# Optimization experiments

Measured on AMD Instinct MI355X. Metric: run time of the kernel, lower is better.

Reference implementation:

```python
import jax, jax.numpy as jnp
import numpy as np

D = 512
A = 256
MAX_DEPTH = 50.0
ANGLE_RANGE = 60.0
SIGMA = 0.5

ANGLES = jnp.linspace(-ANGLE_RANGE / 2, ANGLE_RANGE / 2, A)  # [A]
DEPTHS = jnp.linspace(0.0, MAX_DEPTH, D)                     # [D]
DEG2RAD = np.float32(np.pi / 180.0)


def _generate_prior(p):
    # p: [B, 3] = [theta_a, d, theta_p]
    d = p[:, 1]        # [B]
    theta_p = p[:, 2]  # [B]
    angle_rad = (theta_p[:, None] + ANGLES[None, :]) * DEG2RAD   # [B, A]
    d_theory = d[:, None] / jnp.cos(angle_rad)                   # [B, A]
    valid = (d_theory > 0.0) & (d_theory < MAX_DEPTH)            # [B, A]
    # Gaussian soft-binning over depth: [B, D, A]
    diff = DEPTHS[None, :, None] - d_theory[:, None, :]
    P = jnp.exp(-(diff * diff) / (2.0 * SIGMA * SIGMA))
    P = jnp.where(valid[:, None, :], P, 0.0)
    # per-column (over depth) normalization, skipping empty columns
    col_sum = P.sum(axis=1, keepdims=True)                       # [B, 1, A]
    denom = jnp.where(col_sum > 0.0, col_sum, 1.0)
    return P / denom


def setup_inputs() -> dict:
    key = jax.random.key(0)
    k1, k2, k3, k4, k5, k6 = jax.random.split(key, 6)
    B = 256

    def make_p(ka, kd, kp):
        theta_a = jax.random.uniform(ka, (B,), minval=-30.0, maxval=30.0)
        d = jax.random.uniform(kd, (B,), minval=1.0, maxval=40.0)
        theta_p = jax.random.uniform(kp, (B,), minval=-10.0, maxval=10.0)
        return jnp.stack([theta_a, d, theta_p], axis=1).astype(jnp.float32)

    return {"p": make_p(k1, k2, k3), "p_calib": make_p(k4, k5, k6)}


def reference(p, p_calib):
    P_d = _generate_prior(p)
    P_c = _generate_prior(p_calib)
    return (P_d, P_c)
```

## Files before the change

kernel.cpp:

```cpp
#include <hip/hip_runtime.h>


#define DD 512
#define AA 256

__global__ __launch_bounds__(256) void prior_kernel(const float* __restrict__ p0,
                                                    const float* __restrict__ p1,
                                                    float* __restrict__ out) {
    const int blk = blockIdx.x;
    const int b   = blk & 255;
    const float* __restrict__ pp = (blk < 256) ? p0 : p1;

    __shared__ __align__(16) float dt_s[AA];
    __shared__ __align__(16) float inv_s[AA];

    const float d  = pp[b * 3 + 1];
    const float th = pp[b * 3 + 2];

    const int t = threadIdx.x;

    {
        const int a = t;
        const float ang = -30.0f + (float)a * (60.0f / 255.0f);
        const float rad = (th + ang) * 0.017453292519943295f;
        float dt = d / cosf(rad);
        const bool valid = (dt > 0.0f) && (dt < 50.0f);
        float sum = 0.0f;
        #pragma unroll 8
        for (int j = 0; j < DD; ++j) {
            const float dep  = (float)j * (50.0f / 511.0f);
            const float diff = dep - dt;
            sum += __expf(-2.0f * diff * diff);
        }
        const float den = (sum > 0.0f) ? sum : 1.0f;
        inv_s[a] = valid ? (1.0f / den) : 0.0f;
        dt_s[a]  = valid ? dt : 1.0e9f;
    }
    __syncthreads();

    const int a4   = (t & 63) * 4;
    const int jblk = t >> 6;
    const float4 dtv = *(const float4*)&dt_s[a4];
    const float4 inv = *(const float4*)&inv_s[a4];

    float* __restrict__ outp = out + (size_t)blk * (DD * AA) + a4;
    const int j0 = jblk * (DD / 4);
    #pragma unroll 4
    for (int j = j0; j < j0 + DD / 4; ++j) {
        const float dep = (float)j * (50.0f / 511.0f);
        float4 v;
        float dx = dep - dtv.x; v.x = __expf(-2.0f * dx * dx) * inv.x;
        float dy = dep - dtv.y; v.y = __expf(-2.0f * dy * dy) * inv.y;
        float dz = dep - dtv.z; v.z = __expf(-2.0f * dz * dz) * inv.z;
        float dw = dep - dtv.w; v.w = __expf(-2.0f * dw * dw) * inv.w;
        *(float4*)(outp + (size_t)j * AA) = v;
    }
}

extern "C" void kernel_launch(void* const* d_in, const int* in_sizes, int n_in,
                              void* d_out, int out_size, void* d_ws, size_t ws_size,
                              hipStream_t stream) {
    const float* p0 = (const float*)d_in[0];
    const float* p1 = (const float*)d_in[1];
    float* out = (float*)d_out;
    prior_kernel<<<dim3(2 * 256), dim3(256), 0, stream>>>(p0, p1, out);
}
```

Before: 261.8 us.

## Window Gaussian column sums, fold normalization into exp2, zero-fill outside band

```diff
diff --git a/kernel.cpp b/kernel.cpp
--- a/kernel.cpp
+++ b/kernel.cpp
@@ -3,21 +3,32 @@
 
 #define DD 512
 #define AA 256
+#define DSTEP (50.0f / 511.0f)
+#define K2 (-2.8853900817779268f)
+#define BHW 34
+
+__device__ __forceinline__ float fexp2(float x) { return __builtin_amdgcn_exp2f(x); }
+__device__ __forceinline__ float flog2(float x) { return __builtin_amdgcn_logf(x); }
 
 __global__ __launch_bounds__(256) void prior_kernel(const float* __restrict__ p0,
                                                     const float* __restrict__ p1,
                                                     float* __restrict__ out) {
-    const int blk = blockIdx.x;
-    const int b   = blk & 255;
+    const int bh   = blockIdx.x;
+    const int blk  = bh >> 1;
+    const int half = bh & 1;
+    const int b    = blk & 255;
     const float* __restrict__ pp = (blk < 256) ? p0 : p1;
 
     __shared__ __align__(16) float dt_s[AA];
-    __shared__ __align__(16) float inv_s[AA];
+    __shared__ __align__(16) float li_s[AA];
+    __shared__ int jlo_s, jhi_s;
+
+    const int t = threadIdx.x;
+    if (t == 0) { jlo_s = 1 << 30; jhi_s = -(1 << 30); }
+    __syncthreads();
 
     const float d  = pp[b * 3 + 1];
     const float th = pp[b * 3 + 2];
-
-    const int t = threadIdx.x;
 
     {
         const int a = t;
@@ -25,36 +36,57 @@
         const float rad = (th + ang) * 0.017453292519943295f;
         float dt = d / cosf(rad);
         const bool valid = (dt > 0.0f) && (dt < 50.0f);
-        float sum = 0.0f;
-        #pragma unroll 8
-        for (int j = 0; j < DD; ++j) {
-            const float dep  = (float)j * (50.0f / 511.0f);
-            const float diff = dep - dt;
-            sum += __expf(-2.0f * diff * diff);
+        float li = 0.0f;
+        if (valid) {
+            const int c  = (int)(dt * (511.0f / 50.0f) + 0.5f);
+            const int lo = max(0, c - 32);
+            const int hi = min(DD - 1, c + 32);
+            float sum = 0.0f;
+            for (int j = lo; j <= hi; ++j) {
+                const float dep = (float)j * DSTEP;
+                const float dx  = dep - dt;
+                sum += fexp2(K2 * dx * dx);
+            }
+            li = -flog2(sum);
+            atomicMin(&jlo_s, c);
+            atomicMax(&jhi_s, c);
+        } else {
+            dt = 1.0e5f;
         }
-        const float den = (sum > 0.0f) ? sum : 1.0f;
-        inv_s[a] = valid ? (1.0f / den) : 0.0f;
-        dt_s[a]  = valid ? dt : 1.0e9f;
+        dt_s[a] = dt;
+        li_s[a] = li;
     }
     __syncthreads();
 
-    const int a4   = (t & 63) * 4;
-    const int jblk = t >> 6;
+    const int a4 = (t & 63) * 4;
     const float4 dtv = *(const float4*)&dt_s[a4];
-    const float4 inv = *(const float4*)&inv_s[a4];
+    const float4 liv = *(const float4*)&li_s[a4];
+
+    const int jq0 = half * 256 + (t >> 6) * 64;
+    const int jq1 = jq0 + 64;
+    const int lo = max(jq0, min(jq1, jlo_s - BHW));
+    const int hi = max(lo,  min(jq1, jhi_s + BHW + 1));
 
     float* __restrict__ outp = out + (size_t)blk * (DD * AA) + a4;
-    const int j0 = jblk * (DD / 4);
-    #pragma unroll 4
-    for (int j = j0; j < j0 + DD / 4; ++j) {
-        const float dep = (float)j * (50.0f / 511.0f);
+    const float4 zero = {0.0f, 0.0f, 0.0f, 0.0f};
+
+    for (int j = jq0; j < lo; ++j)
+        *(float4*)(outp + (size_t)j * AA) = zero;
+
+    float jf = (float)lo;
+    for (int j = lo; j < hi; ++j, jf += 1.0f) {
+        const float dep = jf * DSTEP;
         float4 v;
-        float dx = dep - dtv.x; v.x = __expf(-2.0f * dx * dx) * inv.x;
-        float dy = dep - dtv.y; v.y = __expf(-2.0f * dy * dy) * inv.y;
-        float dz = dep - dtv.z; v.z = __expf(-2.0f * dz * dz) * inv.z;
-        float dw = dep - dtv.w; v.w = __expf(-2.0f * dw * dw) * inv.w;
+        float dx;
+        dx = dep - dtv.x; v.x = fexp2(__fmaf_rn(K2 * dx, dx, liv.x));
+        dx = dep - dtv.y; v.y = fexp2(__fmaf_rn(K2 * dx, dx, liv.y));
+        dx = dep - dtv.z; v.z = fexp2(__fmaf_rn(K2 * dx, dx, liv.z));
+        dx = dep - dtv.w; v.w = fexp2(__fmaf_rn(K2 * dx, dx, liv.w));
         *(float4*)(outp + (size_t)j * AA) = v;
     }
+
+    for (int j = hi; j < jq1; ++j)
+        *(float4*)(outp + (size_t)j * AA) = zero;
 }
 
 extern "C" void kernel_launch(void* const* d_in, const int* in_sizes, int n_in,
@@ -63,5 +95,5 @@
     const float* p0 = (const float*)d_in[0];
     const float* p1 = (const float*)d_in[1];
     float* out = (float*)d_out;
-    prior_kernel<<<dim3(2 * 256), dim3(256), 0, stream>>>(p0, p1, out);
+    prior_kernel<<<dim3(2 * 2 * 256), dim3(256), 0, stream>>>(p0, p1, out);
 }
```

Measured after the change: 262.1 us. No clear change (+0.1%).
